# Optimization experiments

Hardware: AMD Instinct MI355X
Metric: run time of the kernel (lower is better)

Reference implementation:

```python
import jax, jax.numpy as jnp
import numpy as np
from jax.scipy.linalg import cho_solve

N, D, T, K, P = 4000, 256, 52, 20, 100
EPS = 1e-8


def _make_kernel(length_scale):
    # RBF kernel over time grid with the same jitter-doubling rule as the torch code.
    t = np.arange(T, dtype=np.float32)
    sq = (t[None, :] - t[:, None]) ** 2
    Kmat = np.exp(-0.5 * sq / np.float32(length_scale) ** 2).astype(np.float32)
    jitter = 1e-4
    eye = np.eye(T, dtype=np.float32)
    while True:
        if np.linalg.cond(Kmat + jitter * eye) < 1e4:
            break
        jitter *= 2
        if jitter > 0.1:
            break
    return jnp.asarray(Kmat + jitter * eye)

K_LAMBDA = _make_kernel(T / 4)  # lambda GP kernel, shared across all k
K_PHI = _make_kernel(T / 3)     # phi GP kernel, shared across all k


def setup_inputs() -> dict:
    key = jax.random.key(0)
    ks = jax.random.split(key, 7)
    lambda_ = jax.random.normal(ks[0], (N, K, T), dtype=jnp.float32)
    phi = jax.random.normal(ks[1], (K, D, T), dtype=jnp.float32)
    gamma = 0.1 * jax.random.normal(ks[2], (P, K), dtype=jnp.float32)
    G = jax.random.normal(ks[3], (N, P), dtype=jnp.float32)
    Y = (jax.random.uniform(ks[4], (N, D, T)) < 0.05).astype(jnp.float32)
    logit_prev_t = jax.random.normal(ks[5], (D, T), dtype=jnp.float32) - 3.0
    event_times = jax.random.randint(ks[6], (N, D), 0, T)
    return dict(lambda_=lambda_, phi=phi, gamma=gamma, G=G, Y=Y,
                logit_prev_t=logit_prev_t, event_times=event_times)


def reference(lambda_, phi, gamma, G, Y, logit_prev_t, event_times):
    # --- forward: softmax over topics, sigmoid disease probs, mixture ---
    theta = jax.nn.softmax(lambda_, axis=1)          # [N,K,T]
    phi_prob = jax.nn.sigmoid(phi)                   # [K,D,T]
    pi = jnp.einsum('nkt,kdt->ndt', theta, phi_prob) # [N,D,T]
    pi = jnp.clip(pi, EPS, 1.0 - EPS)

    # --- survival data loss ---
    tgrid = jnp.arange(T)[None, None, :]             # [1,1,T]
    e = event_times[:, :, None]                      # [N,D,1]
    mask_before = (tgrid < e).astype(pi.dtype)
    mask_at = (tgrid == e).astype(pi.dtype)
    log_pi = jnp.log(pi)
    log_1mpi = jnp.log1p(-pi)
    loss_censored = -jnp.sum(log_1mpi * mask_before)
    loss_event = -jnp.sum(log_pi * mask_at * Y)
    loss_no_event = -jnp.sum(log_1mpi * mask_at * (1.0 - Y))
    data_loss = (loss_censored + loss_event + loss_no_event) / N

    # --- GP prior loss: batched cholesky solves replace per-sample loops ---
    L_lam = jnp.linalg.cholesky(K_LAMBDA)            # [T,T]
    L_phi = jnp.linalg.cholesky(K_PHI)               # [T,T]
    mean_lam = G @ gamma                             # [N,K]
    dev_lam = (lambda_ - mean_lam[:, :, None]).reshape(N * K, T)  # [N*K,T]
    v_lam = cho_solve((L_lam, True), dev_lam.T)      # [T,N*K]
    gp_lambda = 0.5 * jnp.sum(dev_lam.T * v_lam)
    dev_phi = (phi - logit_prev_t[None, :, :]).reshape(K * D, T)  # [K*D,T]
    v_phi = cho_solve((L_phi, True), dev_phi.T)      # [T,K*D]
    gp_phi = 0.5 * jnp.sum(dev_phi.T * v_phi)
    gp_loss = gp_lambda / N + gp_phi / D

    return data_loss + gp_loss
```

## Files before the change

kernel.cpp:

```cpp
#include <hip/hip_runtime.h>
#include <math.h>
#include <string.h>

#define Nn 4000
#define Dd 256
#define Tt 52
#define Kk 20
#define Pp 100
#define CH 4
#define TC 13
#define GRID_D ((Nn / 8) * CH)

#define OFF_W       0
#define OFF_GPART   5408
#define OFF_DLP     5556
#define OFF_CNT     7556
#define OFF_EVP     7560
#define OFF_PHIP    263560
#define OFF_THETA   529800

#define GR_ROWS 128

#define RB_PHIP0   0
#define RB_THETA0  52
#define RB_GPHI0   865
#define RB_GLAM0   885
#define RB_EVY0    1010
#define RB_TOTAL   2010

__global__ __launch_bounds__(256) void prep_kernel(
    const float* __restrict__ lam, const float* __restrict__ phi,
    const float* __restrict__ gamma, const float* __restrict__ G,
    const float* __restrict__ logit_prev, const int* __restrict__ ev,
    const float* __restrict__ Y,
    float* __restrict__ theta_t, float* __restrict__ phip_t,
    unsigned int* __restrict__ evy,
    const float* __restrict__ W, float* __restrict__ gpart,
    unsigned int* __restrict__ cnt) {
    __shared__ float rows[GR_ROWS][56];
    __shared__ float meanv[GR_ROWS];
    __shared__ double redd[256];
    const int bx = blockIdx.x, tid = threadIdx.x;

    if (bx < RB_THETA0) {
        if (bx == 0 && tid == 0) *cnt = 0u;
        int gid = bx * 256 + tid;
        int d = gid / Tt, t = gid - d * Tt;
        float v[Kk];
#pragma unroll
        for (int k = 0; k < Kk; ++k) {
            float x = phi[k * (Dd * Tt) + gid];
            v[k] = 1.f / (1.f + __expf(-x));
        }
#pragma unroll
        for (int k = 0; k < Kk; ++k)
            phip_t[((size_t)t * Kk + k) * Dd + d] = v[k];
        return;
    }
    if (bx < RB_GPHI0) {
        int gid = (bx - RB_THETA0) * 256 + tid;
        if (gid >= Nn * Tt) return;
        int n = gid / Tt, t = gid - n * Tt;
        const float* base = lam + n * Kk * Tt + t;
        float v[Kk];
        float m = -1e30f;
#pragma unroll
        for (int k = 0; k < Kk; ++k) { v[k] = base[k * Tt]; m = fmaxf(m, v[k]); }
        float s = 0.f;
#pragma unroll
        for (int k = 0; k < Kk; ++k) { v[k] = __expf(v[k] - m); s += v[k]; }
        float inv = 1.f / s;
        float* o = theta_t + ((size_t)t * Nn + n) * Kk;
#pragma unroll
        for (int k = 0; k < Kk; ++k) o[k] = v[k] * inv;
        return;
    }
    if (bx < RB_GLAM0) {
        int slot = bx - RB_GPHI0;
        int ta = tid % 13, tb = tid / 13;
        float acc[4][4] = {};
        for (int it = 0; it < 2; ++it) {
            int R0 = (slot * 2 + it) * GR_ROWS;
            __syncthreads();
            for (int idx = tid; idx < GR_ROWS * Tt; idx += 256) {
                int r = idx / Tt, t = idx - r * Tt;
                int R = R0 + r;
                rows[r][t] = phi[R * Tt + t] - logit_prev[(R & 255) * Tt + t];
            }
            __syncthreads();
            if (tb < 13) {
                for (int r = 0; r < GR_ROWS; ++r) {
                    float4 a = *(const float4*)&rows[r][4 * ta];
                    float4 b = *(const float4*)&rows[r][4 * tb];
                    float av[4] = {a.x, a.y, a.z, a.w};
                    float bv[4] = {b.x, b.y, b.z, b.w};
#pragma unroll
                    for (int i = 0; i < 4; ++i)
#pragma unroll
                        for (int j = 0; j < 4; ++j) acc[i][j] += av[i] * bv[j];
                }
            }
        }
        double s = 0.0;
        if (tb < 13)
#pragma unroll
            for (int i = 0; i < 4; ++i)
#pragma unroll
                for (int j = 0; j < 4; ++j)
                    s += (double)acc[i][j] *
                         (double)W[2704 + (4 * ta + i) * Tt + 4 * tb + j];
        redd[tid] = s;
        __syncthreads();
        for (int off = 128; off; off >>= 1) {
            if (tid < off) redd[tid] += redd[tid + off];
            __syncthreads();
        }
        if (tid == 0) gpart[125 + slot] = (float)redd[0];
        return;
    }
    if (bx < RB_EVY0) {
        int slot = bx - RB_GLAM0;
        int ta = tid % 13, tb = tid / 13;
        float acc[4][4] = {};
        for (int it = 0; it < 5; ++it) {
            int R0 = (slot * 5 + it) * GR_ROWS;
            __syncthreads();
            if (tid < GR_ROWS) {
                int R = R0 + tid;
                int n = R / Kk, k = R - n * Kk;
                float m = 0.f;
                for (int p = 0; p < Pp; ++p) m += G[n * Pp + p] * gamma[p * Kk + k];
                meanv[tid] = m;
            }
            __syncthreads();
            for (int idx = tid; idx < GR_ROWS * Tt; idx += 256) {
                int r = idx / Tt, t = idx - r * Tt;
                int R = R0 + r;
                rows[r][t] = lam[R * Tt + t] - meanv[r];
            }
            __syncthreads();
            if (tb < 13) {
                for (int r = 0; r < GR_ROWS; ++r) {
                    float4 a = *(const float4*)&rows[r][4 * ta];
                    float4 b = *(const float4*)&rows[r][4 * tb];
                    float av[4] = {a.x, a.y, a.z, a.w};
                    float bv[4] = {b.x, b.y, b.z, b.w};
#pragma unroll
                    for (int i = 0; i < 4; ++i)
#pragma unroll
                        for (int j = 0; j < 4; ++j) acc[i][j] += av[i] * bv[j];
                }
            }
        }
        double s = 0.0;
        if (tb < 13)
#pragma unroll
            for (int i = 0; i < 4; ++i)
#pragma unroll
                for (int j = 0; j < 4; ++j)
                    s += (double)acc[i][j] *
                         (double)W[(4 * ta + i) * Tt + 4 * tb + j];
        redd[tid] = s;
        __syncthreads();
        for (int off = 128; off; off >>= 1) {
            if (tid < off) redd[tid] += redd[tid + off];
            __syncthreads();
        }
        if (tid == 0) gpart[slot] = (float)redd[0];
        return;
    }
    {
        int idx = bx - RB_EVY0;
        int ng = idx >> 1, half = idx & 1;
        int n0 = ng * 8 + half * 4;
        unsigned a = 0;
#pragma unroll
        for (int g = 0; g < 4; ++g) {
            int nd = (n0 + g) * Dd + tid;
            unsigned e = (unsigned)ev[nd] & 63u;
            float y = __builtin_nontemporal_load(Y + (size_t)nd * Tt + e);
            a |= (e | (y > 0.5f ? 128u : 0u)) << (8 * g);
        }
        evy[((size_t)ng * Dd + tid) * 2 + half] = a;
        return;
    }
}

__global__ __launch_bounds__(256) void data_kernel(const float* __restrict__ theta_t,
                                                   const float* __restrict__ phip_t,
                                                   const uint2* __restrict__ evy,
                                                   float* __restrict__ ws,
                                                   float* __restrict__ out,
                                                   unsigned int* __restrict__ cnt) {
    __shared__ __align__(16) float thS[TC][8][Kk];
    __shared__ float wsum[4];
    __shared__ double redd[256];
    __shared__ int isLast;
    const int tid = threadIdx.x;
    const int d = tid;
    const int ng = blockIdx.x >> 2;
    const int t0 = (blockIdx.x & 3) * TC;
    const int n0 = ng * 8;

    for (int idx = tid; idx < TC * 160; idx += 256) {
        int j = idx / 160, r = idx - j * 160;
        thS[j][r / Kk][r - (r / Kk) * Kk] =
            theta_t[((size_t)(t0 + j) * Nn + n0) * Kk + r];
    }

    uint2 ee = evy[(size_t)ng * Dd + d];
    int e[8];
    float Yv[8], acc[8], pie[8], prod[8];
#pragma unroll
    for (int g = 0; g < 8; ++g) {
        unsigned byte = ((g < 4 ? ee.x : ee.y) >> (8 * (g & 3))) & 255u;
        e[g] = (int)(byte & 63u);
        Yv[g] = (byte & 128u) ? 1.f : 0.f;
        acc[g] = 0.f; prod[g] = 1.f; pie[g] = 0.5f;
    }
    __syncthreads();

    for (int j = 0; j < TC; ++j) {
        int t = t0 + j;
        float pv[Kk];
        const float* pt = phip_t + (size_t)t * (Kk * Dd) + d;
#pragma unroll
        for (int k = 0; k < Kk; ++k) pv[k] = pt[k * Dd];
#pragma unroll
        for (int g = 0; g < 8; ++g) {
            const float4* th = (const float4*)&thS[j][g][0];
            float4 a0 = th[0], a1 = th[1], a2 = th[2], a3 = th[3], a4 = th[4];
            float pi = a0.x * pv[0] + a0.y * pv[1] + a0.z * pv[2] + a0.w * pv[3]
                     + a1.x * pv[4] + a1.y * pv[5] + a1.z * pv[6] + a1.w * pv[7]
                     + a2.x * pv[8] + a2.y * pv[9] + a2.z * pv[10] + a2.w * pv[11]
                     + a3.x * pv[12] + a3.y * pv[13] + a3.z * pv[14] + a3.w * pv[15]
                     + a4.x * pv[16] + a4.y * pv[17] + a4.z * pv[18] + a4.w * pv[19];
            pi = fminf(fmaxf(pi, 1e-8f), 1.0f - 1e-8f);
            prod[g] *= (t <= e[g]) ? (1.f - pi) : 1.f;
            pie[g] = (t == e[g]) ? pi : pie[g];
        }
        if ((j & 3) == 3 || j == TC - 1) {
#pragma unroll
            for (int g = 0; g < 8; ++g) { acc[g] += __logf(prod[g]); prod[g] = 1.f; }
        }
    }
    float tsum = 0.f;
#pragma unroll
    for (int g = 0; g < 8; ++g)
        tsum += acc[g] + Yv[g] * (__logf(pie[g]) - __logf(1.f - pie[g]));
    for (int off = 32; off; off >>= 1) tsum += __shfl_down(tsum, off, 64);
    if ((tid & 63) == 0) wsum[tid >> 6] = tsum;
    __syncthreads();
    if (tid == 0) {
        ws[OFF_DLP + blockIdx.x] = -(wsum[0] + wsum[1] + wsum[2] + wsum[3]);
        __threadfence();
        unsigned prev = atomicAdd(cnt, 1u);
        isLast = (prev == GRID_D - 1) ? 1 : 0;
    }
    __syncthreads();
    if (!isLast) return;

    __threadfence();
    double s = 0.0;
    for (int i = tid; i < 145; i += 256) s += (double)ws[OFF_GPART + i];
    double dl = 0.0;
    for (int i = tid; i < GRID_D; i += 256) dl += (double)ws[OFF_DLP + i];
    s += dl / Nn;
    redd[tid] = s;
    __syncthreads();
    for (int off = 128; off; off >>= 1) {
        if (tid < off) redd[tid] += redd[tid + off];
        __syncthreads();
    }
    if (tid == 0) out[0] = (float)redd[0];
}


static void build_K_f(double ls_in, float Kf[52][52]) {
    float ls = (float)ls_in;
    float ls2 = ls * ls;
    for (int i = 0; i < 52; ++i)
        for (int j = 0; j < 52; ++j) {
            float sq = (float)((i - j) * (i - j));
            float arg = (-0.5f * sq) / ls2;
            Kf[i][j] = expf(arg);
        }
}

static void jacobi_eig(double a[52][52], double ev[52]) {
    const int n = 52;
    for (int sweep = 0; sweep < 100; ++sweep) {
        double off = 0;
        for (int p = 0; p < n - 1; ++p)
            for (int q = p + 1; q < n; ++q) off += a[p][q] * a[p][q];
        if (off < 1e-24) break;
        for (int p = 0; p < n - 1; ++p)
            for (int q = p + 1; q < n; ++q) {
                double apq = a[p][q];
                if (fabs(apq) < 1e-300) continue;
                double th = (a[q][q] - a[p][p]) / (2.0 * apq);
                double t = (th >= 0 ? 1.0 : -1.0) / (fabs(th) + sqrt(th * th + 1.0));
                double c = 1.0 / sqrt(t * t + 1.0), s = t * c;
                for (int i = 0; i < n; ++i) {
                    double aip = a[i][p], aiq = a[i][q];
                    a[i][p] = c * aip - s * aiq;
                    a[i][q] = s * aip + c * aiq;
                }
                for (int i = 0; i < n; ++i) {
                    double api = a[p][i], aqi = a[q][i];
                    a[p][i] = c * api - s * aqi;
                    a[q][i] = s * api + c * aqi;
                }
            }
    }
    for (int i = 0; i < n; ++i) ev[i] = a[i][i];
}

static void build_A(const float Kf[52][52], double jitter, double A[52][52]) {
    float jf = (float)jitter;
    for (int i = 0; i < 52; ++i)
        for (int j = 0; j < 52; ++j) A[i][j] = (double)Kf[i][j];
    for (int i = 0; i < 52; ++i) A[i][i] = (double)(float)(Kf[i][i] + jf);
}

static double cond_of(const float Kf[52][52], double jitter) {
    double A[52][52], ev[52];
    build_A(Kf, jitter, A);
    jacobi_eig(A, ev);
    double mx = 0.0, mn = 1e300;
    for (int i = 0; i < 52; ++i) {
        double a = fabs(ev[i]);
        if (a > mx) mx = a;
        if (a < mn) mn = a;
    }
    if (mn <= 0.0) return 1e300;
    return mx / mn;
}

static double find_jitter(const float Kf[52][52]) {
    double jitter = 1e-4;
    while (true) {
        if (cond_of(Kf, jitter) < 1e4) break;
        jitter *= 2.0;
        if (jitter > 0.1) break;
    }
    return jitter;
}

static void chol_inv_scaled(const float Kf[52][52], double jitter, double scale,
                            float* out) {
    const int n = 52;
    double A[52][52], L[52][52];
    build_A(Kf, jitter, A);
    memset(L, 0, sizeof(L));
    for (int j = 0; j < n; ++j) {
        double s = A[j][j];
        for (int k = 0; k < j; ++k) s -= L[j][k] * L[j][k];
        L[j][j] = sqrt(s);
        for (int i = j + 1; i < n; ++i) {
            double v = A[i][j];
            for (int k = 0; k < j; ++k) v -= L[i][k] * L[j][k];
            L[i][j] = v / L[j][j];
        }
    }
    for (int c = 0; c < n; ++c) {
        double y[52], x[52];
        for (int i = 0; i < n; ++i) {
            double v = (i == c) ? 1.0 : 0.0;
            for (int k = 0; k < i; ++k) v -= L[i][k] * y[k];
            y[i] = v / L[i][i];
        }
        for (int i = n - 1; i >= 0; --i) {
            double v = y[i];
            for (int k = i + 1; k < n; ++k) v -= L[k][i] * x[k];
            x[i] = v / L[i][i];
        }
        for (int i = 0; i < n; ++i) out[i * 52 + c] = (float)(x[i] * scale);
    }
}

struct KinvInit {
    float* w;
    KinvInit() {
        if (hipHostMalloc((void**)&w, 5408 * sizeof(float)) != hipSuccess)
            w = (float*)malloc(5408 * sizeof(float));
        float Kf[52][52];
        build_K_f(52.0 / 4.0, Kf);
        chol_inv_scaled(Kf, find_jitter(Kf), 0.5 / Nn, w);
        build_K_f(52.0 / 3.0, Kf);
        chol_inv_scaled(Kf, find_jitter(Kf), 0.5 / Dd, w + 2704);
    }
};
static KinvInit g_kinv;


extern "C" void kernel_launch(void* const* d_in, const int* in_sizes, int n_in,
                              void* d_out, int out_size, void* d_ws, size_t ws_size,
                              hipStream_t stream) {
    (void)in_sizes; (void)n_in; (void)out_size; (void)ws_size;
    const float* lam        = (const float*)d_in[0];
    const float* phi        = (const float*)d_in[1];
    const float* gamma      = (const float*)d_in[2];
    const float* G          = (const float*)d_in[3];
    const float* Y          = (const float*)d_in[4];
    const float* logit_prev = (const float*)d_in[5];
    const int*   ev         = (const int*)d_in[6];
    float* out = (float*)d_out;
    float* ws  = (float*)d_ws;

    hipMemcpyAsync(ws + OFF_W, g_kinv.w, 5408 * sizeof(float),
                   hipMemcpyHostToDevice, stream);

    prep_kernel<<<RB_TOTAL, 256, 0, stream>>>(
        lam, phi, gamma, G, logit_prev, ev, Y,
        ws + OFF_THETA, ws + OFF_PHIP, (unsigned int*)(ws + OFF_EVP),
        ws + OFF_W, ws + OFF_GPART, (unsigned int*)(ws + OFF_CNT));
    data_kernel<<<GRID_D, 256, 0, stream>>>(
        ws + OFF_THETA, ws + OFF_PHIP, (const uint2*)(ws + OFF_EVP),
        ws, out, (unsigned int*)(ws + OFF_CNT));
}
```

Before: 435.0 us.

## Fuse topic softmax into data kernel, dropping theta workspace round-trip

```diff
diff --git a/kernel.cpp b/kernel.cpp
--- a/kernel.cpp
+++ b/kernel.cpp
@@ -17,24 +17,21 @@
 #define OFF_CNT     7556
 #define OFF_EVP     7560
 #define OFF_PHIP    263560
-#define OFF_THETA   529800
 
 #define GR_ROWS 128
 
 #define RB_PHIP0   0
-#define RB_THETA0  52
-#define RB_GPHI0   865
-#define RB_GLAM0   885
-#define RB_EVY0    1010
-#define RB_TOTAL   2010
+#define RB_GPHI0   52
+#define RB_GLAM0   72
+#define RB_EVY0    197
+#define RB_TOTAL   1197
 
 __global__ __launch_bounds__(256) void prep_kernel(
     const float* __restrict__ lam, const float* __restrict__ phi,
     const float* __restrict__ gamma, const float* __restrict__ G,
     const float* __restrict__ logit_prev, const int* __restrict__ ev,
     const float* __restrict__ Y,
-    float* __restrict__ theta_t, float* __restrict__ phip_t,
-    unsigned int* __restrict__ evy,
+    float* __restrict__ phip_t, unsigned int* __restrict__ evy,
     const float* __restrict__ W, float* __restrict__ gpart,
     unsigned int* __restrict__ cnt) {
     __shared__ float rows[GR_ROWS][56];
@@ -42,7 +39,7 @@
     __shared__ double redd[256];
     const int bx = blockIdx.x, tid = threadIdx.x;
 
-    if (bx < RB_THETA0) {
+    if (bx < RB_GPHI0) {
         if (bx == 0 && tid == 0) *cnt = 0u;
         int gid = bx * 256 + tid;
         int d = gid / Tt, t = gid - d * Tt;
@@ -55,24 +52,6 @@
 #pragma unroll
         for (int k = 0; k < Kk; ++k)
             phip_t[((size_t)t * Kk + k) * Dd + d] = v[k];
-        return;
-    }
-    if (bx < RB_GPHI0) {
-        int gid = (bx - RB_THETA0) * 256 + tid;
-        if (gid >= Nn * Tt) return;
-        int n = gid / Tt, t = gid - n * Tt;
-        const float* base = lam + n * Kk * Tt + t;
-        float v[Kk];
-        float m = -1e30f;
-#pragma unroll
-        for (int k = 0; k < Kk; ++k) { v[k] = base[k * Tt]; m = fmaxf(m, v[k]); }
-        float s = 0.f;
-#pragma unroll
-        for (int k = 0; k < Kk; ++k) { v[k] = __expf(v[k] - m); s += v[k]; }
-        float inv = 1.f / s;
-        float* o = theta_t + ((size_t)t * Nn + n) * Kk;
-#pragma unroll
-        for (int k = 0; k < Kk; ++k) o[k] = v[k] * inv;
         return;
     }
     if (bx < RB_GLAM0) {
@@ -186,13 +165,14 @@
     }
 }
 
-__global__ __launch_bounds__(256) void data_kernel(const float* __restrict__ theta_t,
+__global__ __launch_bounds__(256) void data_kernel(const float* __restrict__ lam,
                                                    const float* __restrict__ phip_t,
                                                    const uint2* __restrict__ evy,
                                                    float* __restrict__ ws,
                                                    float* __restrict__ out,
                                                    unsigned int* __restrict__ cnt) {
     __shared__ __align__(16) float thS[TC][8][Kk];
+    __shared__ float lamS[8][Kk][TC + 1];
     __shared__ float wsum[4];
     __shared__ double redd[256];
     __shared__ int isLast;
@@ -202,10 +182,25 @@
     const int t0 = (blockIdx.x & 3) * TC;
     const int n0 = ng * 8;
 
-    for (int idx = tid; idx < TC * 160; idx += 256) {
-        int j = idx / 160, r = idx - j * 160;
-        thS[j][r / Kk][r - (r / Kk) * Kk] =
-            theta_t[((size_t)(t0 + j) * Nn + n0) * Kk + r];
+    if (tid < 8 * Kk) {
+        int n = tid / Kk, k = tid - n * Kk;
+        const float* src = lam + ((size_t)(n0 + n) * Kk + k) * Tt + t0;
+#pragma unroll
+        for (int j = 0; j < TC; ++j) lamS[n][k][j] = src[j];
+    }
+    __syncthreads();
+    if (tid < 8 * TC) {
+        int n = tid / TC, j = tid - n * TC;
+        float v[Kk];
+        float m = -1e30f;
+#pragma unroll
+        for (int k = 0; k < Kk; ++k) { v[k] = lamS[n][k][j]; m = fmaxf(m, v[k]); }
+        float s = 0.f;
+#pragma unroll
+        for (int k = 0; k < Kk; ++k) { v[k] = __expf(v[k] - m); s += v[k]; }
+        float inv = 1.f / s;
+#pragma unroll
+        for (int k = 0; k < Kk; ++k) thS[j][n][k] = v[k] * inv;
     }
 
     uint2 ee = evy[(size_t)ng * Dd + d];
@@ -413,9 +408,9 @@
 
     prep_kernel<<<RB_TOTAL, 256, 0, stream>>>(
         lam, phi, gamma, G, logit_prev, ev, Y,
-        ws + OFF_THETA, ws + OFF_PHIP, (unsigned int*)(ws + OFF_EVP),
+        ws + OFF_PHIP, (unsigned int*)(ws + OFF_EVP),
         ws + OFF_W, ws + OFF_GPART, (unsigned int*)(ws + OFF_CNT));
     data_kernel<<<GRID_D, 256, 0, stream>>>(
-        ws + OFF_THETA, ws + OFF_PHIP, (const uint2*)(ws + OFF_EVP),
+        lam, ws + OFF_PHIP, (const uint2*)(ws + OFF_EVP),
         ws, out, (unsigned int*)(ws + OFF_CNT));
 }
```

New measurement: 433.9 us, median of 2. No clear change (-0.2%).
